# Kernel optimization log

Measured on AMD Instinct MI355X. Metric: run time of the kernel, lower is better.

The kernel has to match this reference:

```python
import jax, jax.numpy as jnp
import numpy as np

B, N, C, H = 2, 2048, 512, 8
D = C // H  # head_dim = 64


def sparsemax(logits):
    # logits: [..., N]; faithful to torch sparsemax (sort+cumsum+threshold)
    z = logits - jnp.max(logits, axis=-1, keepdims=True)
    sorted_z = -jnp.sort(-z, axis=-1)  # descending
    cssv = jnp.cumsum(sorted_z, axis=-1) - 1.0
    ind = jnp.arange(1, logits.shape[-1] + 1, dtype=logits.dtype)
    cond = sorted_z > cssv / ind
    k = jnp.sum(cond, axis=-1, keepdims=True).astype(jnp.int32)  # support size >=1
    tau = jnp.take_along_axis(cssv, k - 1, axis=-1) / k.astype(logits.dtype)
    return jnp.maximum(z - tau, 0.0)


def setup_inputs() -> dict:
    key = jax.random.key(0)
    ks = jax.random.split(key, 5)
    s = 1.0 / np.sqrt(C)
    return {
        "x": jax.random.normal(ks[0], (B, N, C), jnp.float32),
        "Wq": jax.random.normal(ks[1], (C, C), jnp.float32) * s,
        "bq": jnp.zeros((C,), jnp.float32),
        "Wk": jax.random.normal(ks[2], (C, C), jnp.float32) * s,
        "bk": jnp.zeros((C,), jnp.float32),
        "Wv": jax.random.normal(ks[3], (C, C), jnp.float32) * s,
        "bv": jnp.zeros((C,), jnp.float32),
        "Wo": jax.random.normal(ks[4], (C, C), jnp.float32) * s,
        "bo": jnp.zeros((C,), jnp.float32),
    }


def reference(x, Wq, bq, Wk, bk, Wv, bv, Wo, bo):
    b, n, c = x.shape
    def proj(W, bias):
        y = x @ W.T + bias  # torch Linear: x @ W^T + b
        return y.reshape(b, n, H, D).transpose(0, 2, 1, 3)  # [B,H,N,D]
    q, k, v = proj(Wq, bq), proj(Wk, bk), proj(Wv, bv)
    scores = jnp.einsum("bhqd,bhkd->bhqk", q, k) / jnp.sqrt(jnp.asarray(D, x.dtype))
    attn = sparsemax(scores)  # [B,H,N,N]
    out = jnp.einsum("bhqk,bhkd->bhqd", attn, v)
    out = out.transpose(0, 2, 1, 3).reshape(b, n, c)
    return out @ Wo.T + bo, attn
```

## Files before the change

### kernel.cpp

```cpp
#include <hip/hip_runtime.h>

#define Bv 2
#define Nv 2048
#define Cv 512
#define Hv 8
#define Dv 64
#define CAP 256

typedef __attribute__((ext_vector_type(8))) short s16x8;
typedef __attribute__((ext_vector_type(4))) float f32x4;

__device__ __forceinline__ unsigned short f2bf(float f) {
  union { float f; unsigned u; } x; x.f = f;
  return (unsigned short)((x.u + 0x7fffu + ((x.u >> 16) & 1u)) >> 16);
}
__device__ __forceinline__ float bf2f(unsigned short u) {
  union { unsigned u; float f; } x; x.u = ((unsigned)u) << 16;
  return x.f;
}

__global__ __launch_bounds__(256) void cvt5(
    const float* __restrict__ x, const float* __restrict__ wq,
    const float* __restrict__ wk, const float* __restrict__ wv_,
    const float* __restrict__ wo,
    unsigned short* __restrict__ xb, unsigned short* __restrict__ wqb,
    unsigned short* __restrict__ wkb, unsigned short* __restrict__ wvb,
    unsigned short* __restrict__ wob) {
  const float* s; unsigned short* d; int n;
  switch (blockIdx.y) {
    case 0: s = x;   d = xb;  n = Bv * Nv * Cv; break;
    case 1: s = wq;  d = wqb; n = Cv * Cv; break;
    case 2: s = wk;  d = wkb; n = Cv * Cv; break;
    case 3: s = wv_; d = wvb; n = Cv * Cv; break;
    default: s = wo; d = wob; n = Cv * Cv; break;
  }
  int i = (blockIdx.x * 256 + threadIdx.x) * 4;
  if (i < n) {
    float4 v = *(const float4*)(s + i);
    ushort4 o;
    o.x = f2bf(v.x); o.y = f2bf(v.y); o.z = f2bf(v.z); o.w = f2bf(v.w);
    *(ushort4*)(d + i) = o;
  }
}

__global__ __launch_bounds__(256) void proj_qkv(
    const unsigned short* __restrict__ xb,
    const unsigned short* __restrict__ wqb, const float* __restrict__ bq,
    const unsigned short* __restrict__ wkb, const float* __restrict__ bk,
    const unsigned short* __restrict__ wvb, const float* __restrict__ bv,
    unsigned short* __restrict__ Qbf, unsigned short* __restrict__ Kbf,
    unsigned short* __restrict__ Vbf) {
  const int lane = threadIdx.x & 63;
  const int wv   = threadIdx.x >> 6;
  const int l16  = lane & 15, quad = lane >> 4;
  const int mbase = blockIdx.x * 64 + wv * 16;
  const int nbase = blockIdx.y * 64;
  const int mat   = blockIdx.z;
  const unsigned short* W = (mat == 0) ? wqb : (mat == 1) ? wkb : wvb;
  const float* bias = (mat == 0) ? bq : (mat == 1) ? bk : bv;
  unsigned short* dst = (mat == 0) ? Qbf : (mat == 1) ? Kbf : Vbf;

  f32x4 acc[4] = {};
  for (int kk = 0; kk < Cv; kk += 32) {
    s16x8 a = *(const s16x8*)(xb + (size_t)(mbase + l16) * Cv + kk + quad * 8);
#pragma unroll
    for (int ct = 0; ct < 4; ct++) {
      s16x8 bfr = *(const s16x8*)(W + (size_t)(nbase + ct * 16 + l16) * Cv + kk + quad * 8);
      acc[ct] = __builtin_amdgcn_mfma_f32_16x16x32_bf16(a, bfr, acc[ct], 0, 0, 0);
    }
  }
#pragma unroll
  for (int ct = 0; ct < 4; ct++) {
    int n = nbase + ct * 16 + l16;
    int h = n >> 6, d = n & 63;
    float bb = bias[n];
#pragma unroll
    for (int r = 0; r < 4; r++) {
      int m = mbase + quad * 4 + r;
      int bidx = m >> 11, nn = m & 2047;
      dst[(((size_t)bidx * Hv + h) * Nv + nn) * Dv + d] = f2bf(acc[ct][r] + bb);
    }
  }
}

__global__ __launch_bounds__(256) void attn_sparse(
    const unsigned short* __restrict__ Qbf, const unsigned short* __restrict__ Kbf,
    const unsigned short* __restrict__ Vbf, float* __restrict__ attn_out,
    unsigned short* __restrict__ Obf) {
  __shared__ float rowmax_w[4][16];
  __shared__ float mrow[16];
  __shared__ float candv[16][CAP];
  __shared__ int   candi[16][CAP];
  __shared__ int   cnt[16];
  __shared__ float lo_s[16], hi_s[16], sum_s[16], taud[16];
  __shared__ int   oflow;

  const int lane = threadIdx.x & 63;
  const int wv   = threadIdx.x >> 6;
  const int l16  = lane & 15, quad = lane >> 4;
  const int bh    = blockIdx.x >> 7;
  const int qbase = (blockIdx.x & 127) << 4;
  const int b = bh >> 3, h = bh & 7;

  const unsigned short* Qh = Qbf + (size_t)bh * Nv * Dv;
  const unsigned short* Kh = Kbf + (size_t)bh * Nv * Dv;
  const unsigned short* Vh = Vbf + (size_t)bh * Nv * Dv;
  float* attn_bh = attn_out + (size_t)bh * Nv * Nv;

  if (threadIdx.x < 16) cnt[threadIdx.x] = 0;
  if (threadIdx.x == 0) oflow = 0;

  s16x8 a0 = *(const s16x8*)(Qh + (size_t)(qbase + l16) * Dv + quad * 8);
  s16x8 a1 = *(const s16x8*)(Qh + (size_t)(qbase + l16) * Dv + 32 + quad * 8);

  float rm[4] = {-1e30f, -1e30f, -1e30f, -1e30f};
  for (int t = 0; t < 32; t++) {
    int col0 = (t * 4 + wv) * 16;
    s16x8 b0 = *(const s16x8*)(Kh + (size_t)(col0 + l16) * Dv + quad * 8);
    s16x8 b1 = *(const s16x8*)(Kh + (size_t)(col0 + l16) * Dv + 32 + quad * 8);
    f32x4 c = {};
    c = __builtin_amdgcn_mfma_f32_16x16x32_bf16(a0, b0, c, 0, 0, 0);
    c = __builtin_amdgcn_mfma_f32_16x16x32_bf16(a1, b1, c, 0, 0, 0);
#pragma unroll
    for (int r = 0; r < 4; r++) rm[r] = fmaxf(rm[r], c[r]);
  }
#pragma unroll
  for (int off = 1; off <= 8; off <<= 1)
#pragma unroll
    for (int r = 0; r < 4; r++) rm[r] = fmaxf(rm[r], __shfl_xor(rm[r], off, 64));
  if (l16 == 0) {
#pragma unroll
    for (int r = 0; r < 4; r++) rowmax_w[wv][quad * 4 + r] = rm[r];
  }
  __syncthreads();
  float m[4];
#pragma unroll
  for (int r = 0; r < 4; r++) {
    int row = quad * 4 + r;
    float mm = fmaxf(fmaxf(rowmax_w[0][row], rowmax_w[1][row]),
                     fmaxf(rowmax_w[2][row], rowmax_w[3][row]));
    m[r] = mm * 0.125f;
  }
  if (wv == 0 && l16 == 0) {
#pragma unroll
    for (int r = 0; r < 4; r++) mrow[quad * 4 + r] = m[r];
  }

  for (int t = 0; t < 32; t++) {
    int col0 = (t * 4 + wv) * 16;
    s16x8 b0 = *(const s16x8*)(Kh + (size_t)(col0 + l16) * Dv + quad * 8);
    s16x8 b1 = *(const s16x8*)(Kh + (size_t)(col0 + l16) * Dv + 32 + quad * 8);
    f32x4 c = {};
    c = __builtin_amdgcn_mfma_f32_16x16x32_bf16(a0, b0, c, 0, 0, 0);
    c = __builtin_amdgcn_mfma_f32_16x16x32_bf16(a1, b1, c, 0, 0, 0);
#pragma unroll
    for (int r = 0; r < 4; r++) {
      float val = c[r] * 0.125f;
      if (val > m[r] - 1.0f) {
        int row = quad * 4 + r;
        int pos = atomicAdd(&cnt[row], 1);
        if (pos < CAP) { candv[row][pos] = val; candi[row][pos] = col0 + l16; }
      }
    }
  }
  __syncthreads();
  if (threadIdx.x < 16 && cnt[threadIdx.x] > CAP) oflow = 1;
  __syncthreads();

  float tau[4];
  if (oflow == 0) {
    float cv[4][4], lo[4], hi[4];
#pragma unroll
    for (int i = 0; i < 4; i++) {
      int row = wv * 4 + i;
      int c_ = cnt[row];
#pragma unroll
      for (int j = 0; j < 4; j++) {
        int p = lane + j * 64;
        cv[i][j] = (p < c_) ? candv[row][p] : -1e30f;
      }
      lo[i] = mrow[row] - 1.0f; hi[i] = mrow[row];
    }
    for (int it = 0; it < 22; it++) {
      float mid[4], s[4];
#pragma unroll
      for (int i = 0; i < 4; i++) {
        mid[i] = 0.5f * (lo[i] + hi[i]);
        float ss = 0.0f;
#pragma unroll
        for (int j = 0; j < 4; j++) ss += fmaxf(cv[i][j] - mid[i], 0.0f);
        s[i] = ss;
      }
#pragma unroll
      for (int off = 32; off > 0; off >>= 1)
#pragma unroll
        for (int i = 0; i < 4; i++) s[i] += __shfl_xor(s[i], off, 64);
#pragma unroll
      for (int i = 0; i < 4; i++) {
        if (s[i] > 1.0f) lo[i] = mid[i]; else hi[i] = mid[i];
      }
    }
#pragma unroll
    for (int i = 0; i < 4; i++) tau[i] = 0.5f * (lo[i] + hi[i]);

#pragma unroll
    for (int i = 0; i < 4; i++) {
      int row = wv * 4 + i;
      float* arow = attn_bh + (size_t)(qbase + row) * Nv;
      int c_ = cnt[row];
#pragma unroll
      for (int j = 0; j < 4; j++) {
        int p = lane + j * 64;
        if (p < c_) {
          float v = cv[i][j] - tau[i];
          if (v > 0.0f) arow[candi[row][p]] = v;
        }
      }
    }
  } else {
    if (threadIdx.x < 16) { lo_s[threadIdx.x] = mrow[threadIdx.x] - 1.0f; hi_s[threadIdx.x] = mrow[threadIdx.x]; }
    __syncthreads();
    for (int it = 0; it < 26; it++) {
      if (threadIdx.x < 16) sum_s[threadIdx.x] = 0.0f;
      __syncthreads();
      float part[4] = {0, 0, 0, 0};
      for (int t = 0; t < 32; t++) {
        int col0 = (t * 4 + wv) * 16;
        s16x8 b0 = *(const s16x8*)(Kh + (size_t)(col0 + l16) * Dv + quad * 8);
        s16x8 b1 = *(const s16x8*)(Kh + (size_t)(col0 + l16) * Dv + 32 + quad * 8);
        f32x4 c = {};
        c = __builtin_amdgcn_mfma_f32_16x16x32_bf16(a0, b0, c, 0, 0, 0);
        c = __builtin_amdgcn_mfma_f32_16x16x32_bf16(a1, b1, c, 0, 0, 0);
#pragma unroll
        for (int r = 0; r < 4; r++) {
          int row = quad * 4 + r;
          float mid = 0.5f * (lo_s[row] + hi_s[row]);
          part[r] += fmaxf(c[r] * 0.125f - mid, 0.0f);
        }
      }
#pragma unroll
      for (int off = 1; off <= 8; off <<= 1)
#pragma unroll
        for (int r = 0; r < 4; r++) part[r] += __shfl_xor(part[r], off, 64);
      if (l16 == 0) {
#pragma unroll
        for (int r = 0; r < 4; r++) atomicAdd(&sum_s[quad * 4 + r], part[r]);
      }
      __syncthreads();
      if (threadIdx.x < 16) {
        float mid = 0.5f * (lo_s[threadIdx.x] + hi_s[threadIdx.x]);
        if (sum_s[threadIdx.x] > 1.0f) lo_s[threadIdx.x] = mid; else hi_s[threadIdx.x] = mid;
      }
      __syncthreads();
    }
    if (threadIdx.x < 16) taud[threadIdx.x] = 0.5f * (lo_s[threadIdx.x] + hi_s[threadIdx.x]);
    __syncthreads();
    for (int t = 0; t < 32; t++) {
      int col0 = (t * 4 + wv) * 16;
      s16x8 b0 = *(const s16x8*)(Kh + (size_t)(col0 + l16) * Dv + quad * 8);
      s16x8 b1 = *(const s16x8*)(Kh + (size_t)(col0 + l16) * Dv + 32 + quad * 8);
      f32x4 c = {};
      c = __builtin_amdgcn_mfma_f32_16x16x32_bf16(a0, b0, c, 0, 0, 0);
      c = __builtin_amdgcn_mfma_f32_16x16x32_bf16(a1, b1, c, 0, 0, 0);
#pragma unroll
      for (int r = 0; r < 4; r++) {
        int row = quad * 4 + r;
        attn_bh[(size_t)(qbase + row) * Nv + col0 + l16] =
            fmaxf(c[r] * 0.125f - taud[row], 0.0f);
      }
    }
    __threadfence();
    __syncthreads();
#pragma unroll
    for (int i = 0; i < 4; i++) tau[i] = taud[wv * 4 + i];
  }

  float o[4] = {0, 0, 0, 0};
  if (oflow == 0) {
#pragma unroll
    for (int i = 0; i < 4; i++) {
      int row = wv * 4 + i;
      int c_ = cnt[row] < CAP ? cnt[row] : CAP;
      for (int jj = 0; jj < c_; jj++) {
        float p = candv[row][jj] - tau[i];
        if (p > 0.0f) {
          int k = candi[row][jj];
          o[i] += p * bf2f(Vh[(size_t)k * Dv + lane]);
        }
      }
    }
  } else {
#pragma unroll
    for (int i = 0; i < 4; i++) {
      int row = wv * 4 + i;
      const float* arow = attn_bh + (size_t)(qbase + row) * Nv;
      for (int k = 0; k < Nv; k++) {
        float p = arow[k];
        if (p > 0.0f) o[i] += p * bf2f(Vh[(size_t)k * Dv + lane]);
      }
    }
  }
#pragma unroll
  for (int i = 0; i < 4; i++) {
    int row = wv * 4 + i;
    Obf[((size_t)(b * Nv + qbase + row)) * Cv + h * Dv + lane] = f2bf(o[i]);
  }
}

__global__ __launch_bounds__(256) void proj_out(
    const unsigned short* __restrict__ Obf, const unsigned short* __restrict__ wob,
    const float* __restrict__ bo, float* __restrict__ out) {
  const int lane = threadIdx.x & 63;
  const int wv   = threadIdx.x >> 6;
  const int l16  = lane & 15, quad = lane >> 4;
  const int mbase = blockIdx.x * 64 + wv * 16;
  const int nbase = blockIdx.y * 64;

  f32x4 acc[4] = {};
  for (int kk = 0; kk < Cv; kk += 32) {
    s16x8 a = *(const s16x8*)(Obf + (size_t)(mbase + l16) * Cv + kk + quad * 8);
#pragma unroll
    for (int ct = 0; ct < 4; ct++) {
      s16x8 bfr = *(const s16x8*)(wob + (size_t)(nbase + ct * 16 + l16) * Cv + kk + quad * 8);
      acc[ct] = __builtin_amdgcn_mfma_f32_16x16x32_bf16(a, bfr, acc[ct], 0, 0, 0);
    }
  }
#pragma unroll
  for (int ct = 0; ct < 4; ct++) {
    int n = nbase + ct * 16 + l16;
    float bb = bo[n];
#pragma unroll
    for (int r = 0; r < 4; r++) {
      int m = mbase + quad * 4 + r;
      out[(size_t)m * Cv + n] = acc[ct][r] + bb;
    }
  }
}

extern "C" void kernel_launch(void* const* d_in, const int* in_sizes, int n_in,
                              void* d_out, int out_size, void* d_ws, size_t ws_size,
                              hipStream_t stream) {
  (void)in_sizes; (void)n_in; (void)out_size; (void)ws_size;
  const float* x  = (const float*)d_in[0];
  const float* Wq = (const float*)d_in[1];
  const float* bq = (const float*)d_in[2];
  const float* Wk = (const float*)d_in[3];
  const float* bk = (const float*)d_in[4];
  const float* Wv = (const float*)d_in[5];
  const float* bv = (const float*)d_in[6];
  const float* Wo = (const float*)d_in[7];
  const float* bo = (const float*)d_in[8];

  float* out  = (float*)d_out;
  float* attn = out + (size_t)Bv * Nv * Cv;

  unsigned short* xb  = (unsigned short*)d_ws;
  unsigned short* wqb = xb  + (size_t)Bv * Nv * Cv;
  unsigned short* wkb = wqb + (size_t)Cv * Cv;
  unsigned short* wvb = wkb + (size_t)Cv * Cv;
  unsigned short* wob = wvb + (size_t)Cv * Cv;
  unsigned short* Qbf = wob + (size_t)Cv * Cv;
  unsigned short* Kbf = Qbf + (size_t)Bv * Hv * Nv * Dv;
  unsigned short* Vbf = Kbf + (size_t)Bv * Hv * Nv * Dv;
  unsigned short* Obf = Vbf + (size_t)Bv * Hv * Nv * Dv;

  hipMemsetAsync(attn, 0, (size_t)Bv * Hv * Nv * Nv * sizeof(float), stream);

  cvt5<<<dim3((Bv * Nv * Cv) / 4 / 256, 5), 256, 0, stream>>>(
      x, Wq, Wk, Wv, Wo, xb, wqb, wkb, wvb, wob);
  proj_qkv<<<dim3((Bv * Nv) / 64, Cv / 64, 3), 256, 0, stream>>>(
      xb, wqb, bq, wkb, bk, wvb, bv, Qbf, Kbf, Vbf);
  attn_sparse<<<dim3(Bv * Hv * (Nv / 16)), 256, 0, stream>>>(
      Qbf, Kbf, Vbf, attn, Obf);
  proj_out<<<dim3((Bv * Nv) / 64, Cv / 64), 256, 0, stream>>>(Obf, wob, bo, out);
}
```

Baseline: 557.7 us.

## Fuse attention zero-fill into coalesced dense row writes and drop memset

Drops the separate full-size memset of the attention matrix. Each row is now built densely in shared memory from the sparse candidates and written to global memory with coalesced float4 stores, so the zero-fill pass and the scattered stores go away. The change also shrinks the candidate capacity to 160 and stores indices as 16-bit to cut LDS use, sets a launch-bounds occupancy hint, and unrolls the P·V accumulation. A smaller capacity makes the slow overflow path more likely, and each row write now needs three block-wide barriers.

```diff
diff --git a/kernel.cpp b/kernel.cpp
--- a/kernel.cpp
+++ b/kernel.cpp
@@ -5,7 +5,7 @@
 #define Cv 512
 #define Hv 8
 #define Dv 64
-#define CAP 256
+#define CAP 160
 
 typedef __attribute__((ext_vector_type(8))) short s16x8;
 typedef __attribute__((ext_vector_type(4))) float f32x4;
@@ -83,17 +83,19 @@
   }
 }
 
-__global__ __launch_bounds__(256) void attn_sparse(
+__global__ __launch_bounds__(256, 6) void attn_sparse(
     const unsigned short* __restrict__ Qbf, const unsigned short* __restrict__ Kbf,
     const unsigned short* __restrict__ Vbf, float* __restrict__ attn_out,
     unsigned short* __restrict__ Obf) {
   __shared__ float rowmax_w[4][16];
   __shared__ float mrow[16];
   __shared__ float candv[16][CAP];
-  __shared__ int   candi[16][CAP];
+  __shared__ unsigned short candi[16][CAP];
   __shared__ int   cnt[16];
+  __shared__ float taus[16];
   __shared__ float lo_s[16], hi_s[16], sum_s[16], taud[16];
   __shared__ int   oflow;
+  __shared__ float4 dense4[512];
 
   const int lane = threadIdx.x & 63;
   const int wv   = threadIdx.x >> 6;
@@ -159,7 +161,10 @@
       if (val > m[r] - 1.0f) {
         int row = quad * 4 + r;
         int pos = atomicAdd(&cnt[row], 1);
-        if (pos < CAP) { candv[row][pos] = val; candi[row][pos] = col0 + l16; }
+        if (pos < CAP) {
+          candv[row][pos] = val;
+          candi[row][pos] = (unsigned short)(col0 + l16);
+        }
       }
     }
   }
@@ -167,15 +172,14 @@
   if (threadIdx.x < 16 && cnt[threadIdx.x] > CAP) oflow = 1;
   __syncthreads();
 
-  float tau[4];
   if (oflow == 0) {
-    float cv[4][4], lo[4], hi[4];
+    float cv[4][3], lo[4], hi[4], tau[4];
 #pragma unroll
     for (int i = 0; i < 4; i++) {
       int row = wv * 4 + i;
       int c_ = cnt[row];
 #pragma unroll
-      for (int j = 0; j < 4; j++) {
+      for (int j = 0; j < 3; j++) {
         int p = lane + j * 64;
         cv[i][j] = (p < c_) ? candv[row][p] : -1e30f;
       }
@@ -188,7 +192,7 @@
         mid[i] = 0.5f * (lo[i] + hi[i]);
         float ss = 0.0f;
 #pragma unroll
-        for (int j = 0; j < 4; j++) ss += fmaxf(cv[i][j] - mid[i], 0.0f);
+        for (int j = 0; j < 3; j++) ss += fmaxf(cv[i][j] - mid[i], 0.0f);
         s[i] = ss;
       }
 #pragma unroll
@@ -201,21 +205,58 @@
       }
     }
 #pragma unroll
-    for (int i = 0; i < 4; i++) tau[i] = 0.5f * (lo[i] + hi[i]);
-
-#pragma unroll
-    for (int i = 0; i < 4; i++) {
-      int row = wv * 4 + i;
+    for (int i = 0; i < 4; i++) {
+      tau[i] = 0.5f * (lo[i] + hi[i]);
+      if (lane == 0) taus[wv * 4 + i] = tau[i];
+    }
+    __syncthreads();
+
+    float* dense = (float*)dense4;
+    const float4 z4 = make_float4(0.f, 0.f, 0.f, 0.f);
+    for (int row = 0; row < 16; row++) {
+      dense4[threadIdx.x * 2]     = z4;
+      dense4[threadIdx.x * 2 + 1] = z4;
+      __syncthreads();
+      int c_ = cnt[row];
+      if (threadIdx.x < c_)
+        dense[candi[row][threadIdx.x]] =
+            fmaxf(candv[row][threadIdx.x] - taus[row], 0.0f);
+      __syncthreads();
+      float4 d0 = dense4[threadIdx.x];
+      float4 d1 = dense4[256 + threadIdx.x];
       float* arow = attn_bh + (size_t)(qbase + row) * Nv;
+      *(float4*)(arow + threadIdx.x * 4) = d0;
+      *(float4*)(arow + 1024 + threadIdx.x * 4) = d1;
+      __syncthreads();
+    }
+
+    float o[4] = {0, 0, 0, 0};
+#pragma unroll
+    for (int i = 0; i < 4; i++) {
+      int row = wv * 4 + i;
       int c_ = cnt[row];
-#pragma unroll
-      for (int j = 0; j < 4; j++) {
-        int p = lane + j * 64;
-        if (p < c_) {
-          float v = cv[i][j] - tau[i];
-          if (v > 0.0f) arow[candi[row][p]] = v;
-        }
-      }
+      int jj = 0;
+      for (; jj + 4 <= c_; jj += 4) {
+        float p0 = candv[row][jj + 0] - tau[i]; int k0 = candi[row][jj + 0];
+        float p1 = candv[row][jj + 1] - tau[i]; int k1 = candi[row][jj + 1];
+        float p2 = candv[row][jj + 2] - tau[i]; int k2 = candi[row][jj + 2];
+        float p3 = candv[row][jj + 3] - tau[i]; int k3 = candi[row][jj + 3];
+        float v0 = bf2f(Vh[(size_t)k0 * Dv + lane]);
+        float v1 = bf2f(Vh[(size_t)k1 * Dv + lane]);
+        float v2 = bf2f(Vh[(size_t)k2 * Dv + lane]);
+        float v3 = bf2f(Vh[(size_t)k3 * Dv + lane]);
+        o[i] += fmaxf(p0, 0.0f) * v0 + fmaxf(p1, 0.0f) * v1 +
+                fmaxf(p2, 0.0f) * v2 + fmaxf(p3, 0.0f) * v3;
+      }
+      for (; jj < c_; jj++) {
+        float p = fmaxf(candv[row][jj] - tau[i], 0.0f);
+        o[i] += p * bf2f(Vh[(size_t)candi[row][jj] * Dv + lane]);
+      }
+    }
+#pragma unroll
+    for (int i = 0; i < 4; i++) {
+      int row = wv * 4 + i;
+      Obf[((size_t)(b * Nv + qbase + row)) * Cv + h * Dv + lane] = f2bf(o[i]);
     }
   } else {
     if (threadIdx.x < 16) { lo_s[threadIdx.x] = mrow[threadIdx.x] - 1.0f; hi_s[threadIdx.x] = mrow[threadIdx.x]; }
@@ -271,25 +312,7 @@
     }
     __threadfence();
     __syncthreads();
-#pragma unroll
-    for (int i = 0; i < 4; i++) tau[i] = taud[wv * 4 + i];
-  }
-
-  float o[4] = {0, 0, 0, 0};
-  if (oflow == 0) {
-#pragma unroll
-    for (int i = 0; i < 4; i++) {
-      int row = wv * 4 + i;
-      int c_ = cnt[row] < CAP ? cnt[row] : CAP;
-      for (int jj = 0; jj < c_; jj++) {
-        float p = candv[row][jj] - tau[i];
-        if (p > 0.0f) {
-          int k = candi[row][jj];
-          o[i] += p * bf2f(Vh[(size_t)k * Dv + lane]);
-        }
-      }
-    }
-  } else {
+    float o[4] = {0, 0, 0, 0};
 #pragma unroll
     for (int i = 0; i < 4; i++) {
       int row = wv * 4 + i;
@@ -299,11 +322,11 @@
         if (p > 0.0f) o[i] += p * bf2f(Vh[(size_t)k * Dv + lane]);
       }
     }
-  }
-#pragma unroll
-  for (int i = 0; i < 4; i++) {
-    int row = wv * 4 + i;
-    Obf[((size_t)(b * Nv + qbase + row)) * Cv + h * Dv + lane] = f2bf(o[i]);
+#pragma unroll
+    for (int i = 0; i < 4; i++) {
+      int row = wv * 4 + i;
+      Obf[((size_t)(b * Nv + qbase + row)) * Cv + h * Dv + lane] = f2bf(o[i]);
+    }
   }
 }
 
@@ -362,9 +385,7 @@
   unsigned short* Qbf = wob + (size_t)Cv * Cv;
   unsigned short* Kbf = Qbf + (size_t)Bv * Hv * Nv * Dv;
   unsigned short* Vbf = Kbf + (size_t)Bv * Hv * Nv * Dv;
-  unsigned short* Obf = Vbf + (size_t)Bv * Hv * Nv * Dv;
-
-  hipMemsetAsync(attn, 0, (size_t)Bv * Hv * Nv * Nv * sizeof(float), stream);
+  unsigned short* Obf = xb;
 
   cvt5<<<dim3((Bv * Nv * Cv) / 4 / 256, 5), 256, 0, stream>>>(
       x, Wq, Wk, Wv, Wo, xb, wqb, wkb, wvb, wob);
```

Measured after the change: 1.400 ms. +150.9%, slower.

## Fuse row-max into candidate pass and write dense attention rows from compact buffers

Applied to the files above, without the earlier changes.

Replaces the separate row-max QK pass with a single pass. It keeps a running per-row max as an order-preserving integer key updated with atomicMax, and admits candidates against that running threshold. The memset of the full attention matrix and the scattered writes are replaced by a compact per-row candidate buffer (probability and ushort index) plus a new kernel that builds each dense row in shared memory and stores it with coalesced float4 writes. Obf reuses the x bf16 buffer. The looser running threshold admits extra early candidates, which raises the chance of overflowing CAP and falling into the slow dense fallback path.

```diff
diff --git a/kernel.cpp b/kernel.cpp
--- a/kernel.cpp
+++ b/kernel.cpp
@@ -17,6 +17,14 @@
 __device__ __forceinline__ float bf2f(unsigned short u) {
   union { unsigned u; float f; } x; x.u = ((unsigned)u) << 16;
   return x.f;
+}
+__device__ __forceinline__ unsigned fkey(float f) {
+  unsigned u = __float_as_uint(f);
+  return (u & 0x80000000u) ? ~u : (u | 0x80000000u);
+}
+__device__ __forceinline__ float funkey(unsigned k) {
+  unsigned u = (k & 0x80000000u) ? (k ^ 0x80000000u) : ~k;
+  return __uint_as_float(u);
 }
 
 __global__ __launch_bounds__(256) void cvt5(
@@ -86,11 +94,12 @@
 __global__ __launch_bounds__(256) void attn_sparse(
     const unsigned short* __restrict__ Qbf, const unsigned short* __restrict__ Kbf,
     const unsigned short* __restrict__ Vbf, float* __restrict__ attn_out,
-    unsigned short* __restrict__ Obf) {
-  __shared__ float rowmax_w[4][16];
-  __shared__ float mrow[16];
+    unsigned short* __restrict__ Obf,
+    float* __restrict__ candp_g, unsigned short* __restrict__ candi_g,
+    int* __restrict__ cnt_g) {
+  __shared__ unsigned rowkey[16];
   __shared__ float candv[16][CAP];
-  __shared__ int   candi[16][CAP];
+  __shared__ unsigned short candi[16][CAP];
   __shared__ int   cnt[16];
   __shared__ float lo_s[16], hi_s[16], sum_s[16], taud[16];
   __shared__ int   oflow;
@@ -107,13 +116,16 @@
   const unsigned short* Vh = Vbf + (size_t)bh * Nv * Dv;
   float* attn_bh = attn_out + (size_t)bh * Nv * Nv;
 
-  if (threadIdx.x < 16) cnt[threadIdx.x] = 0;
+  if (threadIdx.x < 16) {
+    cnt[threadIdx.x] = 0;
+    rowkey[threadIdx.x] = fkey(-1e30f);
+  }
   if (threadIdx.x == 0) oflow = 0;
+  __syncthreads();
 
   s16x8 a0 = *(const s16x8*)(Qh + (size_t)(qbase + l16) * Dv + quad * 8);
   s16x8 a1 = *(const s16x8*)(Qh + (size_t)(qbase + l16) * Dv + 32 + quad * 8);
 
-  float rm[4] = {-1e30f, -1e30f, -1e30f, -1e30f};
   for (int t = 0; t < 32; t++) {
     int col0 = (t * 4 + wv) * 16;
     s16x8 b0 = *(const s16x8*)(Kh + (size_t)(col0 + l16) * Dv + quad * 8);
@@ -122,44 +134,18 @@
     c = __builtin_amdgcn_mfma_f32_16x16x32_bf16(a0, b0, c, 0, 0, 0);
     c = __builtin_amdgcn_mfma_f32_16x16x32_bf16(a1, b1, c, 0, 0, 0);
 #pragma unroll
-    for (int r = 0; r < 4; r++) rm[r] = fmaxf(rm[r], c[r]);
-  }
-#pragma unroll
-  for (int off = 1; off <= 8; off <<= 1)
-#pragma unroll
-    for (int r = 0; r < 4; r++) rm[r] = fmaxf(rm[r], __shfl_xor(rm[r], off, 64));
-  if (l16 == 0) {
-#pragma unroll
-    for (int r = 0; r < 4; r++) rowmax_w[wv][quad * 4 + r] = rm[r];
-  }
-  __syncthreads();
-  float m[4];
-#pragma unroll
-  for (int r = 0; r < 4; r++) {
-    int row = quad * 4 + r;
-    float mm = fmaxf(fmaxf(rowmax_w[0][row], rowmax_w[1][row]),
-                     fmaxf(rowmax_w[2][row], rowmax_w[3][row]));
-    m[r] = mm * 0.125f;
-  }
-  if (wv == 0 && l16 == 0) {
-#pragma unroll
-    for (int r = 0; r < 4; r++) mrow[quad * 4 + r] = m[r];
-  }
-
-  for (int t = 0; t < 32; t++) {
-    int col0 = (t * 4 + wv) * 16;
-    s16x8 b0 = *(const s16x8*)(Kh + (size_t)(col0 + l16) * Dv + quad * 8);
-    s16x8 b1 = *(const s16x8*)(Kh + (size_t)(col0 + l16) * Dv + 32 + quad * 8);
-    f32x4 c = {};
-    c = __builtin_amdgcn_mfma_f32_16x16x32_bf16(a0, b0, c, 0, 0, 0);
-    c = __builtin_amdgcn_mfma_f32_16x16x32_bf16(a1, b1, c, 0, 0, 0);
-#pragma unroll
     for (int r = 0; r < 4; r++) {
       float val = c[r] * 0.125f;
-      if (val > m[r] - 1.0f) {
-        int row = quad * 4 + r;
+      int row = quad * 4 + r;
+      unsigned cur = rowkey[row];
+      if (fkey(val + 1.0f) > cur) {
         int pos = atomicAdd(&cnt[row], 1);
-        if (pos < CAP) { candv[row][pos] = val; candi[row][pos] = col0 + l16; }
+        if (pos < CAP) {
+          candv[row][pos] = val;
+          candi[row][pos] = (unsigned short)(col0 + l16);
+        }
+        unsigned k = fkey(val);
+        if (k > cur) atomicMax(&rowkey[row], k);
       }
     }
   }
@@ -167,9 +153,8 @@
   if (threadIdx.x < 16 && cnt[threadIdx.x] > CAP) oflow = 1;
   __syncthreads();
 
-  float tau[4];
   if (oflow == 0) {
-    float cv[4][4], lo[4], hi[4];
+    float cv[4][4], lo[4], hi[4], tau[4];
 #pragma unroll
     for (int i = 0; i < 4; i++) {
       int row = wv * 4 + i;
@@ -179,7 +164,8 @@
         int p = lane + j * 64;
         cv[i][j] = (p < c_) ? candv[row][p] : -1e30f;
       }
-      lo[i] = mrow[row] - 1.0f; hi[i] = mrow[row];
+      float mx = funkey(rowkey[row]);
+      lo[i] = mx - 1.0f; hi[i] = mx;
     }
     for (int it = 0; it < 22; it++) {
       float mid[4], s[4];
@@ -206,19 +192,36 @@
 #pragma unroll
     for (int i = 0; i < 4; i++) {
       int row = wv * 4 + i;
-      float* arow = attn_bh + (size_t)(qbase + row) * Nv;
+      size_t rowg = (size_t)blockIdx.x * 16 + row;
       int c_ = cnt[row];
-#pragma unroll
-      for (int j = 0; j < 4; j++) {
-        int p = lane + j * 64;
-        if (p < c_) {
-          float v = cv[i][j] - tau[i];
-          if (v > 0.0f) arow[candi[row][p]] = v;
-        }
-      }
+      for (int jj = lane; jj < c_; jj += 64) {
+        candp_g[rowg * CAP + jj] = fmaxf(candv[row][jj] - tau[i], 0.0f);
+        candi_g[rowg * CAP + jj] = candi[row][jj];
+      }
+      if (lane == 0) cnt_g[rowg] = c_;
+    }
+
+    float o[4] = {0, 0, 0, 0};
+#pragma unroll
+    for (int i = 0; i < 4; i++) {
+      int row = wv * 4 + i;
+      int c_ = cnt[row];
+      for (int jj = 0; jj < c_; jj++) {
+        float p = fmaxf(candv[row][jj] - tau[i], 0.0f);
+        o[i] += p * bf2f(Vh[(size_t)candi[row][jj] * Dv + lane]);
+      }
+    }
+#pragma unroll
+    for (int i = 0; i < 4; i++) {
+      int row = wv * 4 + i;
+      Obf[((size_t)(b * Nv + qbase + row)) * Cv + h * Dv + lane] = f2bf(o[i]);
     }
   } else {
-    if (threadIdx.x < 16) { lo_s[threadIdx.x] = mrow[threadIdx.x] - 1.0f; hi_s[threadIdx.x] = mrow[threadIdx.x]; }
+    if (threadIdx.x < 16) {
+      float mx = funkey(rowkey[threadIdx.x]);
+      lo_s[threadIdx.x] = mx - 1.0f; hi_s[threadIdx.x] = mx;
+      cnt_g[(size_t)blockIdx.x * 16 + threadIdx.x] = -1;
+    }
     __syncthreads();
     for (int it = 0; it < 26; it++) {
       if (threadIdx.x < 16) sum_s[threadIdx.x] = 0.0f;
@@ -271,25 +274,7 @@
     }
     __threadfence();
     __syncthreads();
-#pragma unroll
-    for (int i = 0; i < 4; i++) tau[i] = taud[wv * 4 + i];
-  }
-
-  float o[4] = {0, 0, 0, 0};
-  if (oflow == 0) {
-#pragma unroll
-    for (int i = 0; i < 4; i++) {
-      int row = wv * 4 + i;
-      int c_ = cnt[row] < CAP ? cnt[row] : CAP;
-      for (int jj = 0; jj < c_; jj++) {
-        float p = candv[row][jj] - tau[i];
-        if (p > 0.0f) {
-          int k = candi[row][jj];
-          o[i] += p * bf2f(Vh[(size_t)k * Dv + lane]);
-        }
-      }
-    }
-  } else {
+    float o[4] = {0, 0, 0, 0};
 #pragma unroll
     for (int i = 0; i < 4; i++) {
       int row = wv * 4 + i;
@@ -299,12 +284,35 @@
         if (p > 0.0f) o[i] += p * bf2f(Vh[(size_t)k * Dv + lane]);
       }
     }
-  }
-#pragma unroll
-  for (int i = 0; i < 4; i++) {
-    int row = wv * 4 + i;
-    Obf[((size_t)(b * Nv + qbase + row)) * Cv + h * Dv + lane] = f2bf(o[i]);
-  }
+#pragma unroll
+    for (int i = 0; i < 4; i++) {
+      int row = wv * 4 + i;
+      Obf[((size_t)(b * Nv + qbase + row)) * Cv + h * Dv + lane] = f2bf(o[i]);
+    }
+  }
+}
+
+__global__ __launch_bounds__(64) void attn_write(
+    const float* __restrict__ candp_g, const unsigned short* __restrict__ candi_g,
+    const int* __restrict__ cnt_g, float* __restrict__ attn_out) {
+  __shared__ float dense[Nv];
+  const size_t rowg = blockIdx.x;
+  const int t = threadIdx.x;
+  const int c_ = cnt_g[rowg];
+  if (c_ < 0) return;
+
+  float4* d4 = (float4*)dense;
+  const float4 z4 = make_float4(0.f, 0.f, 0.f, 0.f);
+#pragma unroll
+  for (int j = 0; j < 8; j++) d4[j * 64 + t] = z4;
+  __syncthreads();
+  for (int jj = t; jj < c_; jj += 64)
+    dense[candi_g[rowg * CAP + jj]] = candp_g[rowg * CAP + jj];
+  __syncthreads();
+  float* arow = attn_out + rowg * Nv;
+#pragma unroll
+  for (int j = 0; j < 8; j++)
+    *(float4*)(arow + (j * 64 + t) * 4) = d4[j * 64 + t];
 }
 
 __global__ __launch_bounds__(256) void proj_out(
@@ -354,6 +362,8 @@
   float* out  = (float*)d_out;
   float* attn = out + (size_t)Bv * Nv * Cv;
 
+  const size_t NROWS = (size_t)Bv * Hv * Nv;
+
   unsigned short* xb  = (unsigned short*)d_ws;
   unsigned short* wqb = xb  + (size_t)Bv * Nv * Cv;
   unsigned short* wkb = wqb + (size_t)Cv * Cv;
@@ -362,15 +372,18 @@
   unsigned short* Qbf = wob + (size_t)Cv * Cv;
   unsigned short* Kbf = Qbf + (size_t)Bv * Hv * Nv * Dv;
   unsigned short* Vbf = Kbf + (size_t)Bv * Hv * Nv * Dv;
-  unsigned short* Obf = Vbf + (size_t)Bv * Hv * Nv * Dv;
-
-  hipMemsetAsync(attn, 0, (size_t)Bv * Hv * Nv * Nv * sizeof(float), stream);
+  unsigned short* end16 = Vbf + (size_t)Bv * Hv * Nv * Dv;
+  float*          candp = (float*)end16;
+  unsigned short* candi = (unsigned short*)(candp + NROWS * CAP);
+  int*            cntg  = (int*)(candi + NROWS * CAP);
+  unsigned short* Obf = xb;
 
   cvt5<<<dim3((Bv * Nv * Cv) / 4 / 256, 5), 256, 0, stream>>>(
       x, Wq, Wk, Wv, Wo, xb, wqb, wkb, wvb, wob);
   proj_qkv<<<dim3((Bv * Nv) / 64, Cv / 64, 3), 256, 0, stream>>>(
       xb, wqb, bq, wkb, bk, wvb, bv, Qbf, Kbf, Vbf);
   attn_sparse<<<dim3(Bv * Hv * (Nv / 16)), 256, 0, stream>>>(
-      Qbf, Kbf, Vbf, attn, Obf);
+      Qbf, Kbf, Vbf, attn, Obf, candp, candi, cntg);
+  attn_write<<<dim3((unsigned)NROWS), 64, 0, stream>>>(candp, candi, cntg, attn);
   proj_out<<<dim3((Bv * Nv) / 64, Cv / 64), 256, 0, stream>>>(Obf, wob, bo, out);
 }
```

New measurement: 1.452 ms. 2.6x slower.
